# Optimization experiments

Hardware: AMD Instinct MI355X
Metric: run time of the kernel (lower is better)

Reference implementation:

```python
import jax, jax.numpy as jnp
import numpy as np

B, S, D, H, E = 2, 512, 768, 12, 8
FF = 4 * D
HD = D // H


def setup_inputs() -> dict:
    key = jax.random.key(0)
    ks = jax.random.split(key, 12)
    s = 0.02
    return {
        "x": jax.random.normal(ks[0], (B, S, D), jnp.float32),
        "ln1_g": jnp.ones((D,), jnp.float32),
        "ln1_b": jnp.zeros((D,), jnp.float32),
        "ln2_g": jnp.ones((D,), jnp.float32),
        "ln2_b": jnp.zeros((D,), jnp.float32),
        "in_proj_w": jax.random.normal(ks[1], (3 * D, D), jnp.float32) * s,
        "in_proj_b": jax.random.normal(ks[2], (3 * D,), jnp.float32) * s,
        "out_proj_w": jax.random.normal(ks[3], (D, D), jnp.float32) * s,
        "out_proj_b": jax.random.normal(ks[4], (D,), jnp.float32) * s,
        "router_w": jax.random.normal(ks[5], (E, D), jnp.float32) * s,
        "router_b": jax.random.normal(ks[6], (E,), jnp.float32) * s,
        "w1": jax.random.normal(ks[7], (E, D, FF), jnp.float32) * s,
        "b1": jax.random.normal(ks[8], (E, FF), jnp.float32) * s,
        "w2": jax.random.normal(ks[9], (E, FF, D), jnp.float32) * s,
        "b2": jax.random.normal(ks[10], (E, D), jnp.float32) * s,
    }


def _layernorm(x, g, b, eps=1e-5):
    mu = x.mean(-1, keepdims=True)
    var = ((x - mu) ** 2).mean(-1, keepdims=True)
    return (x - mu) * jax.lax.rsqrt(var + eps) * g + b


def _forward(x, ln1_g, ln1_b, ln2_g, ln2_b, in_proj_w, in_proj_b,
             out_proj_w, out_proj_b, router_w, router_b, w1, b1, w2, b2):
    # --- self-attention sublayer (pre-norm per torch module ordering) ---
    h = _layernorm(x, ln1_g, ln1_b)
    qkv = h @ in_proj_w.T + in_proj_b                     # [B,S,3D]
    q, k, v = jnp.split(qkv, 3, axis=-1)
    to_heads = lambda t: t.reshape(B, S, H, HD).transpose(0, 2, 1, 3)  # [B,H,S,hd]
    q, k, v = to_heads(q), to_heads(k), to_heads(v)
    scores = jnp.einsum('bhqd,bhkd->bhqk', q, k) / np.float32(np.sqrt(HD))
    attn = jax.nn.softmax(scores, axis=-1)
    o = jnp.einsum('bhqk,bhkd->bhqd', attn, v).transpose(0, 2, 1, 3).reshape(B, S, D)
    o = o @ out_proj_w.T + out_proj_b
    x = x + o
    # --- MoE sublayer: top-2 routing, renormalized gates ---
    h2 = _layernorm(x, ln2_g, ln2_b)
    t = h2.reshape(-1, D)                                  # [T,D]
    logits = t @ router_w.T + router_b                     # [T,E]
    probs = jax.nn.softmax(logits, axis=-1)
    top_v, top_i = jax.lax.top_k(probs, 2)                 # [T,2]
    top_v = top_v / top_v.sum(-1, keepdims=True)
    # per-(token, expert) combine weight (0 if expert not in token's top-2)
    comb = jnp.sum(jax.nn.one_hot(top_i, E, dtype=probs.dtype) * top_v[..., None], axis=1)  # [T,E]
    # dense grouped-FFN: every token through every expert, zero-weighted combine
    hid = jax.nn.gelu(jnp.einsum('td,edf->tef', t, w1) + b1, approximate=False)  # exact GELU as torch
    y = jnp.einsum('tef,efd->ted', hid, w2) + b2           # [T,E,D]
    moe = jnp.einsum('te,ted->td', comb, y).reshape(B, S, D)
    return x + moe


def reference(x, ln1_g, ln1_b, ln2_g, ln2_b, in_proj_w, in_proj_b,
              out_proj_w, out_proj_b, router_w, router_b, w1, b1, w2, b2):
    return _forward(x, ln1_g, ln1_b, ln2_g, ln2_b, in_proj_w, in_proj_b,
                    out_proj_w, out_proj_b, router_w, router_b, w1, b1, w2, b2)
```

## Files before the change

### kernel.cpp

```cpp
#include <hip/hip_runtime.h>
#include <hip/hip_bf16.h>

#define BATCH 2
#define SEQ 512
#define DIM 768
#define HEADS 12
#define NEXP 8
#define FFDIM 3072
#define HDIM 64
#define NTOK (BATCH*SEQ)
#define NENT (2*NTOK)
#define YPS ((long)NENT * DIM)

typedef __hip_bfloat16 bf16;
typedef __attribute__((ext_vector_type(8))) short s8v;
typedef __attribute__((ext_vector_type(4))) float f4v;

typedef __attribute__((address_space(1))) const unsigned char gas_u8;
typedef __attribute__((address_space(3))) unsigned char las_u8;
__device__ __forceinline__ void gload16(const void* g, void* l) {
    __builtin_amdgcn_global_load_lds((gas_u8*)g, (las_u8*)l, 16, 0, 0);
}

__device__ __forceinline__ float bfbits2f(unsigned hi16) {
    union { unsigned u; float f; } c; c.u = hi16; return c.f;
}
__device__ __forceinline__ unsigned short bf16bits(float f) {
    bf16 h = __float2bfloat16(f);
    return *reinterpret_cast<unsigned short*>(&h);
}

__global__ __launch_bounds__(256) void ln_kernel(const float* __restrict__ x,
                                                 const float* __restrict__ g,
                                                 const float* __restrict__ b,
                                                 bf16* __restrict__ outb) {
    int t = blockIdx.x;
    const float* xr = x + (long)t * DIM;
    int tid = threadIdx.x;
    float v0 = xr[tid], v1 = xr[tid + 256], v2 = xr[tid + 512];
    float s = v0 + v1 + v2;
    __shared__ float red[4];
    #pragma unroll
    for (int o = 32; o; o >>= 1) s += __shfl_xor(s, o);
    if ((tid & 63) == 0) red[tid >> 6] = s;
    __syncthreads();
    s = red[0] + red[1] + red[2] + red[3];
    float mu = s * (1.f / DIM);
    float d0 = v0 - mu, d1 = v1 - mu, d2 = v2 - mu;
    float q = d0*d0 + d1*d1 + d2*d2;
    __shared__ float red2[4];
    #pragma unroll
    for (int o = 32; o; o >>= 1) q += __shfl_xor(q, o);
    if ((tid & 63) == 0) red2[tid >> 6] = q;
    __syncthreads();
    q = red2[0] + red2[1] + red2[2] + red2[3];
    float rstd = rsqrtf(q * (1.f / DIM) + 1e-5f);
    bf16* ob = outb + (long)t * DIM;
    ob[tid]       = __float2bfloat16(d0 * rstd * g[tid]       + b[tid]);
    ob[tid + 256] = __float2bfloat16(d1 * rstd * g[tid + 256] + b[tid + 256]);
    ob[tid + 512] = __float2bfloat16(d2 * rstd * g[tid + 512] + b[tid + 512]);
}

__global__ __launch_bounds__(256) void ln2x1_kernel(const float* __restrict__ x,
                                                    const float* __restrict__ out_b,
                                                    const float* __restrict__ op,
                                                    const float* __restrict__ g,
                                                    const float* __restrict__ b,
                                                    float* __restrict__ x1,
                                                    float* __restrict__ t2,
                                                    bf16* __restrict__ t2b) {
    int t = blockIdx.x;
    long base = (long)t * DIM;
    int tid = threadIdx.x;
    const long TDl = (long)NTOK * DIM;
    float v[3];
    #pragma unroll
    for (int i = 0; i < 3; ++i) {
        long idx = base + tid + i * 256;
        v[i] = x[idx] + out_b[tid + i * 256] + op[idx] + op[idx + TDl];
        x1[idx] = v[i];
    }
    float s = v[0] + v[1] + v[2];
    __shared__ float red[4];
    #pragma unroll
    for (int o = 32; o; o >>= 1) s += __shfl_xor(s, o);
    if ((tid & 63) == 0) red[tid >> 6] = s;
    __syncthreads();
    s = red[0] + red[1] + red[2] + red[3];
    float mu = s * (1.f / DIM);
    float d[3];
    float q = 0.f;
    #pragma unroll
    for (int i = 0; i < 3; ++i) { d[i] = v[i] - mu; q += d[i] * d[i]; }
    __shared__ float red2[4];
    #pragma unroll
    for (int o = 32; o; o >>= 1) q += __shfl_xor(q, o);
    if ((tid & 63) == 0) red2[tid >> 6] = q;
    __syncthreads();
    q = red2[0] + red2[1] + red2[2] + red2[3];
    float rstd = rsqrtf(q * (1.f / DIM) + 1e-5f);
    #pragma unroll
    for (int i = 0; i < 3; ++i) {
        long idx = base + tid + i * 256;
        float o = d[i] * rstd * g[tid + i * 256] + b[tid + i * 256];
        t2[idx] = o;
        t2b[idx] = __float2bfloat16(o);
    }
}

template<int WM, int WN, bool GROUPED, bool GELU, int OUTMODE>
__global__ __launch_bounds__(256) void mfma_gemm(
    const bf16* __restrict__ A, const bf16* __restrict__ B,
    const float* __restrict__ bias, const float* __restrict__ resid,
    void* __restrict__ Cv,
    int M, int N, int K, int lda, int ldb, int ldc,
    int zdiv, int ksplit,
    long a_hi, long a_lo, long b_hi, long b_lo, long c_hi, long c_lo,
    long bias_stride, const int* __restrict__ grp_off, float alpha)
{
    constexpr int BM = 32 * WM, BN = 32 * WN;
    constexpr int ACH = BM * 4;
    constexpr int BCH = BN * 4;

    int z = blockIdx.z;
    int ze = z / ksplit, ks = z % ksplit;
    int kper = K / ksplit;
    long aoff, boff, coff;
    int m_count = M;
    if (GROUPED) {
        int m0 = grp_off[ze], m1 = grp_off[ze + 1];
        m_count = m1 - m0;
        if ((int)blockIdx.y * BM >= m_count) return;
        aoff = (long)m0 * lda;
        coff = (long)m0 * ldc;
        boff = (long)ze * b_hi;
    } else {
        int zh = ze / zdiv, zl = ze % zdiv;
        aoff = zh * a_hi + zl * a_lo;
        boff = zh * b_hi + zl * b_lo;
        coff = zh * c_hi + zl * c_lo;
    }
    const short* Ag = (const short*)(A + aoff);
    const short* Bg = (const short*)(B + boff);
    const float* biasp = bias ? bias + (long)ze * bias_stride : nullptr;
    float* Cf = (float*)Cv + coff;
    bf16*  Cb = (bf16*)Cv + coff;

    __shared__ short As[BM * 32];
    __shared__ short Bs[BN * 32];

    int tid = threadIdx.x;
    int wv = tid >> 6, ln = tid & 63;
    int wr = wv >> 1, wc = wv & 1;
    int fr = ln & 15, fq = ln >> 4;
    int bm = blockIdx.y * BM, bn = blockIdx.x * BN;

    f4v acc[WM][WN] = {};

    for (int k0 = ks * kper; k0 < (ks + 1) * kper; k0 += 32) {
        #pragma unroll
        for (int is = 0; is < ACH / 256; ++is) {
            int c = is * 256 + wv * 64 + ln;
            int m = c >> 2, kq = c & 3;
            int qg = kq ^ ((m >> 1) & 3);
            gload16(Ag + (long)(bm + m) * lda + k0 + qg * 8,
                    &As[(is * 256 + wv * 64) * 8]);
        }
        if constexpr (ACH % 256) {
            if (tid < ACH % 256) {
                int c = (ACH / 256) * 256 + tid;
                int m = c >> 2, kq = c & 3;
                int qg = kq ^ ((m >> 1) & 3);
                gload16(Ag + (long)(bm + m) * lda + k0 + qg * 8,
                        &As[((ACH / 256) * 256 + wv * 64) * 8]);
            }
        }
        #pragma unroll
        for (int is = 0; is < BCH / 256; ++is) {
            int c = is * 256 + wv * 64 + ln;
            int m = c >> 2, kq = c & 3;
            int qg = kq ^ ((m >> 1) & 3);
            gload16(Bg + (long)(bn + m) * ldb + k0 + qg * 8,
                    &Bs[(is * 256 + wv * 64) * 8]);
        }
        if constexpr (BCH % 256) {
            if (tid < BCH % 256) {
                int c = (BCH / 256) * 256 + tid;
                int m = c >> 2, kq = c & 3;
                int qg = kq ^ ((m >> 1) & 3);
                gload16(Bg + (long)(bn + m) * ldb + k0 + qg * 8,
                        &Bs[((BCH / 256) * 256 + wv * 64) * 8]);
            }
        }
        __syncthreads();
        s8v av[WM], bv[WN];
        #pragma unroll
        for (int i = 0; i < WM; ++i) {
            int row = wr * (WM * 16) + i * 16 + fr;
            av[i] = *(const s8v*)&As[row * 32 + (fq ^ ((row >> 1) & 3)) * 8];
        }
        #pragma unroll
        for (int j = 0; j < WN; ++j) {
            int row = wc * (WN * 16) + j * 16 + fr;
            bv[j] = *(const s8v*)&Bs[row * 32 + (fq ^ ((row >> 1) & 3)) * 8];
        }
        #pragma unroll
        for (int i = 0; i < WM; ++i)
            #pragma unroll
            for (int j = 0; j < WN; ++j)
                acc[i][j] = __builtin_amdgcn_mfma_f32_16x16x32_bf16(av[i], bv[j], acc[i][j], 0, 0, 0);
        __syncthreads();
    }

    #pragma unroll
    for (int i = 0; i < WM; ++i) {
        #pragma unroll
        for (int r = 0; r < 4; ++r) {
            int row = bm + wr * (WM * 16) + i * 16 + fq * 4 + r;
            if (GROUPED && row >= m_count) continue;
            #pragma unroll
            for (int j = 0; j < WN; ++j) {
                int col = bn + wc * (WN * 16) + j * 16 + fr;
                if (col < N) {
                    float v = acc[i][j][r] * alpha;
                    if (OUTMODE == 2) {
                        atomicAdd(&Cf[(long)row * ldc + col], v);
                    } else {
                        if (biasp) v += biasp[col];
                        if (GELU) v = 0.5f * v * (1.f + erff(v * 0.70710678118654752f));
                        if (resid) v += resid[(long)row * ldc + col];
                        if (OUTMODE == 1) Cb[(long)row * ldc + col] = __float2bfloat16(v);
                        else              Cf[(long)row * ldc + col] = v;
                    }
                }
            }
        }
    }
}

template<int FM, int FN, int XT, int YCAP, int KS, bool GELU, int OUTMODE, bool GATHER>
__global__ __launch_bounds__(256) void moe_gemm(
    const bf16* __restrict__ A, const bf16* __restrict__ B,
    const float* __restrict__ bias, void* __restrict__ Cv,
    int lda, int Nt, int ldc, int Ktot, long b_hi, long bias_stride,
    const int* __restrict__ grp_off, const int* __restrict__ entry_tok,
    int N, long pstride)
{
    static_assert(OUTMODE != 1 || KS == 1, "plain bf16 store requires no split-K");
    constexpr int BM = FM * 32, BN = FN * 32;
    constexpr int GA = BM / 64;
    constexpr int GB = BN / 64;
    constexpr int G = GA + GB;

    int bid = blockIdx.x;
    int e = bid & 7;
    int r = bid >> 3;
    int xt = r % XT; r /= XT;
    int yt = r % YCAP;
    int ks = r / YCAP;
    int m0 = grp_off[e], m1 = grp_off[e + 1];
    int m_count = m1 - m0;
    int bm = yt * BM;
    if (bm >= m_count) return;
    int bn = xt * BN;
    int kper = Ktot / KS;

    const short* Ag = (const short*)A + (GATHER ? 0 : (long)m0 * lda);
    const short* Bg = (const short*)(B + (long)e * b_hi);
    const float* biasp = bias ? bias + (long)e * bias_stride : nullptr;
    float* Cf = (float*)Cv + (long)m0 * ldc + (long)ks * pstride;
    bf16*  Cb = (bf16*)Cv + (long)m0 * ldc;

    __shared__ short As[3][BM * 32];
    __shared__ short Bs[3][BN * 32];

    int tid = threadIdx.x;
    int wv = tid >> 6, ln = tid & 63;
    int wr = wv >> 1, wc = wv & 1;
    int fr = ln & 15, fq = ln >> 4;

    long arow[GA];
    #pragma unroll
    for (int is = 0; is < GA; ++is) {
        int c = is * 256 + wv * 64 + ln;
        int m = c >> 2;
        if (GATHER) {
            int gi = m0 + bm + m;
            arow[is] = (long)entry_tok[gi < NENT ? gi : NENT - 1] * lda;
        } else {
            arow[is] = (long)(bm + m) * lda;
        }
    }

    f4v acc[FM][FN] = {};

    auto stage = [&](int buf, int k0) {
        #pragma unroll
        for (int is = 0; is < GA; ++is) {
            int c = is * 256 + wv * 64 + ln;
            int m = c >> 2, q = c & 3;
            int qg = q ^ ((m >> 1) & 3);
            gload16(Ag + arow[is] + k0 + qg * 8,
                    &As[buf][(is * 256 + wv * 64) * 8]);
        }
        #pragma unroll
        for (int is = 0; is < GB; ++is) {
            int c = is * 256 + wv * 64 + ln;
            int n = c >> 2, q = c & 3;
            int qg = q ^ ((n >> 1) & 3);
            gload16(Bg + ((long)(k0 >> 3) + qg) * Nt * 8 + (long)(bn + n) * 8,
                    &Bs[buf][(is * 256 + wv * 64) * 8]);
        }
    };

    int kbeg = ks * kper;
    int nit = kper / 32;
    stage(0, kbeg);
    if (nit > 1) stage(1, kbeg + 32);

    for (int it = 0; it < nit; ++it) {
        if (it + 1 < nit) asm volatile("s_waitcnt vmcnt(%0)" :: "i"(G) : "memory");
        else              asm volatile("s_waitcnt vmcnt(0)" ::: "memory");
        __builtin_amdgcn_s_barrier();
        if (it + 2 < nit) stage((it + 2) % 3, kbeg + (it + 2) * 32);
        int cur = it % 3;
        __builtin_amdgcn_s_setprio(1);
        {
            s8v av[FM], bv[FN];
            #pragma unroll
            for (int i = 0; i < FM; ++i) {
                int row = wr * (FM * 16) + i * 16 + fr;
                av[i] = *(const s8v*)&As[cur][row * 32 + (fq ^ ((row >> 1) & 3)) * 8];
            }
            #pragma unroll
            for (int j = 0; j < FN; ++j) {
                int row = wc * (FN * 16) + j * 16 + fr;
                bv[j] = *(const s8v*)&Bs[cur][row * 32 + (fq ^ ((row >> 1) & 3)) * 8];
            }
            #pragma unroll
            for (int i = 0; i < FM; ++i)
                #pragma unroll
                for (int j = 0; j < FN; ++j)
                    acc[i][j] = __builtin_amdgcn_mfma_f32_16x16x32_bf16(av[i], bv[j], acc[i][j], 0, 0, 0);
        }
        __builtin_amdgcn_s_setprio(0);
    }

    #pragma unroll
    for (int i = 0; i < FM; ++i) {
        #pragma unroll
        for (int rr = 0; rr < 4; ++rr) {
            int row = bm + wr * (FM * 16) + i * 16 + fq * 4 + rr;
            if (row >= m_count) continue;
            #pragma unroll
            for (int j = 0; j < FN; ++j) {
                int col = bn + wc * (FN * 16) + j * 16 + fr;
                float v = acc[i][j][rr];
                if (OUTMODE == 0) {
                    Cf[(long)row * ldc + col] = v;
                } else {
                    if (biasp) v += biasp[col];
                    if (GELU) v = 0.5f * v * (1.f + erff(v * 0.70710678118654752f));
                    Cb[(long)row * ldc + col] = __float2bfloat16(v);
                }
            }
        }
    }
}

__global__ __launch_bounds__(256) void softmax512b(const bf16* __restrict__ s,
                                                   bf16* __restrict__ attn) {
    long row = (long)blockIdx.x * 4 + (threadIdx.x >> 6);
    int ln = threadIdx.x & 63;
    const unsigned* p = (const unsigned*)(s + row * 512);
    uint4 v = *(const uint4*)(p + ln * 4);
    unsigned u[4] = {v.x, v.y, v.z, v.w};
    float f[8];
    #pragma unroll
    for (int j = 0; j < 4; ++j) {
        f[2*j]   = bfbits2f(u[j] << 16);
        f[2*j+1] = bfbits2f(u[j] & 0xffff0000u);
    }
    float m = f[0];
    #pragma unroll
    for (int j = 1; j < 8; ++j) m = fmaxf(m, f[j]);
    #pragma unroll
    for (int o = 32; o; o >>= 1) m = fmaxf(m, __shfl_xor(m, o));
    float e[8], ssum = 0.f;
    #pragma unroll
    for (int j = 0; j < 8; ++j) { e[j] = expf(f[j] - m); ssum += e[j]; }
    #pragma unroll
    for (int o = 32; o; o >>= 1) ssum += __shfl_xor(ssum, o);
    float inv = 1.f / ssum;
    unsigned w[4];
    #pragma unroll
    for (int j = 0; j < 4; ++j) {
        bf16 lo = __float2bfloat16(e[2*j] * inv);
        bf16 hi = __float2bfloat16(e[2*j+1] * inv);
        w[j] = ((unsigned)*(unsigned short*)&hi << 16) | *(unsigned short*)&lo;
    }
    uint4 o4; o4.x = w[0]; o4.y = w[1]; o4.z = w[2]; o4.w = w[3];
    *(uint4*)((unsigned*)(attn + row * 512) + ln * 4) = o4;
}

__global__ __launch_bounds__(256) void vt_kernel(const bf16* __restrict__ qkvb,
                                                 bf16* __restrict__ vt) {
    int st = blockIdx.x;
    int z = blockIdx.y;
    int b = z / HEADS, h = z % HEADS;
    __shared__ short tile[64][65];
    int t = threadIdx.x;
    int d = t & 63, s0 = t >> 6;
    const short* q = (const short*)qkvb;
    #pragma unroll
    for (int i = 0; i < 16; ++i) {
        int s = st * 64 + s0 + i * 4;
        tile[s0 + i * 4][d] = q[(long)(b * SEQ + s) * 2304 + 2 * DIM + h * HDIM + d];
    }
    __syncthreads();
    short* o = (short*)vt;
    #pragma unroll
    for (int i = 0; i < 16; ++i) {
        int d2 = (t >> 6) + i * 4;
        o[(long)(z * 64 + d2) * 512 + st * 64 + (t & 63)] = tile[t & 63][d2];
    }
}

__global__ __launch_bounds__(256) void wtrans2_kernel(const float* __restrict__ w1,
                                                      bf16* __restrict__ w1t,
                                                      const float* __restrict__ w2,
                                                      bf16* __restrict__ w2t) {
    int id = blockIdx.x;
    const float* in; bf16* out; int C, e, ct, rt;
    if (id < 4608) {
        e = id / 576; int rem = id % 576; ct = rem / 12; rt = rem % 12;
        in = w1; out = w1t; C = FFDIM;
    } else {
        id -= 4608;
        e = id / 576; int rem = id % 576; ct = rem / 48; rt = rem % 48;
        in = w2; out = w2t; C = DIM;
    }
    long ibase = (long)e * DIM * FFDIM;
    int rt0 = rt * 64, ct0 = ct * 64;
    __shared__ float tile[64][65];
    int t = threadIdx.x;
    {
        int q = t >> 4, cq = t & 15;
        #pragma unroll
        for (int i = 0; i < 4; ++i) {
            int row = q + i * 16;
            float4 v = *(const float4*)&in[ibase + (long)(rt0 + row) * C + ct0 + cq * 4];
            tile[row][cq * 4]     = v.x;
            tile[row][cq * 4 + 1] = v.y;
            tile[row][cq * 4 + 2] = v.z;
            tile[row][cq * 4 + 3] = v.w;
        }
    }
    __syncthreads();
    {
        int kb2 = t >> 6, n = t & 63;
        #pragma unroll
        for (int i = 0; i < 2; ++i) {
            int kblk = kb2 + 4 * i;
            unsigned w[4];
            #pragma unroll
            for (int j = 0; j < 4; ++j) {
                w[j] = ((unsigned)bf16bits(tile[kblk * 8 + 2 * j + 1][n]) << 16)
                     | bf16bits(tile[kblk * 8 + 2 * j][n]);
            }
            uint4 u; u.x = w[0]; u.y = w[1]; u.z = w[2]; u.w = w[3];
            *(uint4*)&out[ibase + ((long)(rt0 >> 3) + kblk) * C * 8 + (long)(ct0 + n) * 8] = u;
        }
    }
}

__global__ __launch_bounds__(256) void cvt2_kernel(const float* __restrict__ a, long na,
                                                   const float* __restrict__ b, long nb,
                                                   bf16* __restrict__ oa,
                                                   bf16* __restrict__ ob) {
    long i = ((long)blockIdx.x * 256 + threadIdx.x) * 4;
    const float* src; bf16* dst; long idx;
    if (i < na) { src = a; dst = oa; idx = i; }
    else if (i < na + nb) { src = b; dst = ob; idx = i - na; }
    else return;
    float4 v = *(const float4*)(src + idx);
    dst[idx]     = __float2bfloat16(v.x);
    dst[idx + 1] = __float2bfloat16(v.y);
    dst[idx + 2] = __float2bfloat16(v.z);
    dst[idx + 3] = __float2bfloat16(v.w);
}

__global__ __launch_bounds__(64) void router_kernel(const float* __restrict__ t2,
                                                    const float* __restrict__ rw,
                                                    const float* __restrict__ rb,
                                                    int* __restrict__ e_sel,
                                                    float* __restrict__ w_sel) {
    int t = blockIdx.x;
    int lane = threadIdx.x;
    const float* tr = t2 + (long)t * DIM;
    float tv[12];
    #pragma unroll
    for (int i = 0; i < 12; ++i) tv[i] = tr[lane + 64 * i];
    float logits[NEXP];
    #pragma unroll
    for (int e = 0; e < NEXP; ++e) {
        const float* wr = rw + (long)e * DIM;
        float s = 0.f;
        #pragma unroll
        for (int i = 0; i < 12; ++i) s += tv[i] * wr[lane + 64 * i];
        #pragma unroll
        for (int o = 32; o; o >>= 1) s += __shfl_xor(s, o);
        logits[e] = s + rb[e];
    }
    if (lane == 0) {
        int e0 = -1, e1 = -1;
        float l0 = -1e30f, l1 = -1e30f;
        #pragma unroll
        for (int e = 0; e < NEXP; ++e) {
            float l = logits[e];
            if (l > l0) { l1 = l0; e1 = e0; l0 = l; e0 = e; }
            else if (l > l1) { l1 = l; e1 = e; }
        }
        float p1 = expf(l1 - l0);
        float inv = 1.f / (1.f + p1);
        e_sel[t * 2] = e0;  e_sel[t * 2 + 1] = e1;
        w_sel[t * 2] = inv; w_sel[t * 2 + 1] = p1 * inv;
    }
}

__global__ __launch_bounds__(1024) void build_lists(const int* __restrict__ e_sel,
                                                    int* __restrict__ entry_tok,
                                                    int* __restrict__ pos,
                                                    int* __restrict__ grp_off) {
    __shared__ int cnt[NEXP];
    __shared__ int off[NEXP + 1];
    __shared__ int cur[NEXP];
    int tid = threadIdx.x;
    if (tid < NEXP) cnt[tid] = 0;
    __syncthreads();
    for (int i = tid; i < NENT; i += 1024) atomicAdd(&cnt[e_sel[i]], 1);
    __syncthreads();
    if (tid == 0) {
        off[0] = 0;
        for (int e = 0; e < NEXP; ++e) off[e + 1] = off[e] + cnt[e];
        for (int e = 0; e < NEXP; ++e) cur[e] = off[e];
    }
    __syncthreads();
    for (int i = tid; i < NENT; i += 1024) {
        int e = e_sel[i];
        int p = atomicAdd(&cur[e], 1);
        entry_tok[p] = i >> 1;
        pos[i] = p;
    }
    if (tid < NEXP + 1) grp_off[tid] = off[tid];
}

__global__ __launch_bounds__(256) void combine_kernel(const float* __restrict__ x1,
                                                      const float* __restrict__ ypart,
                                                      const float* __restrict__ b2,
                                                      const int* __restrict__ pos,
                                                      const int* __restrict__ e_sel,
                                                      const float* __restrict__ wsel,
                                                      float* __restrict__ out) {
    long i4 = (long)blockIdx.x * 256 + threadIdx.x;
    if (i4 >= (long)NTOK * DIM / 4) return;
    int t = (int)(i4 / 192), d4 = (int)(i4 % 192);
    const float4* x1v = (const float4*)x1;
    const float4* ypv = (const float4*)ypart;
    const float4* b2v = (const float4*)b2;
    float4 v = x1v[i4];
    #pragma unroll
    for (int s = 0; s < 2; ++s) {
        long base = (long)pos[t * 2 + s] * 192 + d4;
        float4 y = b2v[(long)e_sel[t * 2 + s] * 192 + d4];
        #pragma unroll
        for (int ks = 0; ks < 4; ++ks) {
            float4 pp = ypv[base + ks * (YPS / 4)];
            y.x += pp.x; y.y += pp.y; y.z += pp.z; y.w += pp.w;
        }
        float w = wsel[t * 2 + s];
        v.x += w * y.x; v.y += w * y.y; v.z += w * y.z; v.w += w * y.w;
    }
    ((float4*)out)[i4] = v;
}

extern "C" void kernel_launch(void* const* d_in, const int* in_sizes, int n_in,
                              void* d_out, int out_size, void* d_ws, size_t ws_size,
                              hipStream_t stream) {
    const float* x        = (const float*)d_in[0];
    const float* ln1_g    = (const float*)d_in[1];
    const float* ln1_b    = (const float*)d_in[2];
    const float* ln2_g    = (const float*)d_in[3];
    const float* ln2_b    = (const float*)d_in[4];
    const float* in_w     = (const float*)d_in[5];
    const float* in_b     = (const float*)d_in[6];
    const float* out_w    = (const float*)d_in[7];
    const float* out_b    = (const float*)d_in[8];
    const float* router_w = (const float*)d_in[9];
    const float* router_b = (const float*)d_in[10];
    const float* w1       = (const float*)d_in[11];
    const float* b1       = (const float*)d_in[12];
    const float* w2       = (const float*)d_in[13];
    const float* b2       = (const float*)d_in[14];
    float* out = (float*)d_out;

    const long TD = (long)NTOK * DIM;
    char* p = (char*)d_ws;
    size_t off = 0;
    auto alloc = [&](size_t bytes) -> void* {
        void* r = p + off; off += (bytes + 255) & ~(size_t)255; return r;
    };
    bf16*  h_b    = (bf16*)alloc(TD * 2);
    bf16*  in_wb  = (bf16*)alloc(2304L * 768 * 2);
    bf16*  qkv_b  = (bf16*)alloc(1024L * 2304 * 2);
    bf16*  out_wb = (bf16*)alloc(768L * 768 * 2);
    bf16*  vt_b   = (bf16*)alloc((24L * 64 + 64) * 512 * 2);
    bf16*  oat_b  = (bf16*)alloc(TD * 2);
    float* opart  = (float*)alloc(2 * TD * 4);
    float* x1     = (float*)alloc(TD * 4);
    float* t2     = (float*)alloc(TD * 4);
    bf16*  t2b    = (bf16*)alloc((NTOK + 256L) * DIM * 2);
    bf16*  w1t    = (bf16*)alloc(8L * 3072 * 768 * 2);
    bf16*  w2t    = (bf16*)alloc(8L * 768 * 3072 * 2);
    bf16*  hid    = (bf16*)alloc((2048L + 256) * 3072 * 2);
    float* ypart  = (float*)alloc(4 * YPS * 4);
    int*   e_sel     = (int*)alloc(NENT * 4);
    float* w_sel     = (float*)alloc(NENT * 4);
    int*   entry_tok = (int*)alloc(NENT * 4);
    int*   pos       = (int*)alloc(NENT * 4);
    int*   grp_off   = (int*)alloc(64);
    bf16* scores = w1t;
    bf16* attn   = (bf16*)((char*)w1t + 24L * 512 * 512 * 2);

    ln_kernel<<<NTOK, 256, 0, stream>>>(x, ln1_g, ln1_b, h_b);
    cvt2_kernel<<<2304, 256, 0, stream>>>(in_w, 2304L * 768, out_w, 768L * 768,
                                          in_wb, out_wb);
    mfma_gemm<2, 2, false, false, 1><<<dim3(36, 16, 1), 256, 0, stream>>>(
        h_b, in_wb, in_b, nullptr, qkv_b,
        NTOK, 3 * DIM, DIM, DIM, DIM, 3 * DIM,
        1, 1, 0, 0, 0, 0, 0, 0, 0, nullptr, 1.f);
    mfma_gemm<2, 4, false, false, 1><<<dim3(4, 8, 24), 256, 0, stream>>>(
        qkv_b, qkv_b + DIM, nullptr, nullptr, scores,
        SEQ, SEQ, HDIM, 3 * DIM, 3 * DIM, SEQ,
        HEADS, 1, (long)SEQ * 3 * DIM, HDIM, (long)SEQ * 3 * DIM, HDIM,
        (long)HEADS * SEQ * SEQ, (long)SEQ * SEQ,
        0, nullptr, 0.125f);
    softmax512b<<<24 * SEQ / 4, 256, 0, stream>>>(scores, attn);
    vt_kernel<<<dim3(8, 24), 256, 0, stream>>>(qkv_b, vt_b);
    mfma_gemm<1, 2, false, false, 1><<<dim3(1, 16, 24), 256, 0, stream>>>(
        attn, vt_b, nullptr, nullptr, oat_b,
        SEQ, HDIM, SEQ, SEQ, SEQ, DIM,
        HEADS, 1, (long)HEADS * SEQ * SEQ, (long)SEQ * SEQ,
        (long)HEADS * HDIM * SEQ, (long)HDIM * SEQ,
        (long)SEQ * DIM, HDIM,
        0, nullptr, 1.f);
    mfma_gemm<2, 2, false, false, 0><<<dim3(12, 16, 2), 256, 0, stream>>>(
        oat_b, out_wb, nullptr, nullptr, opart,
        NTOK, DIM, 384, DIM, DIM, DIM,
        2, 1, 0, 384, 0, 384, 0, TD, 0, nullptr, 1.f);
    ln2x1_kernel<<<NTOK, 256, 0, stream>>>(x, out_b, opart, ln2_g, ln2_b,
                                           x1, t2, t2b);
    router_kernel<<<NTOK, 64, 0, stream>>>(t2, router_w, router_b, e_sel, w_sel);
    build_lists<<<1, 1024, 0, stream>>>(e_sel, entry_tok, pos, grp_off);
    wtrans2_kernel<<<9216, 256, 0, stream>>>(w1, w1t, w2, w2t);
    moe_gemm<4, 4, 24, 8, 1, true, 1, true><<<8 * 24 * 8, 256, 0, stream>>>(
        t2b, w1t, b1, hid,
        DIM, FFDIM, FFDIM, DIM, (long)FFDIM * DIM, FFDIM, grp_off, entry_tok,
        FFDIM, 0);
    moe_gemm<4, 4, 6, 8, 4, false, 0, false><<<8 * 6 * 8 * 4, 256, 0, stream>>>(
        hid, w2t, nullptr, ypart,
        FFDIM, DIM, DIM, FFDIM, (long)FFDIM * DIM, 0, grp_off, nullptr,
        DIM, YPS);
    combine_kernel<<<768, 256, 0, stream>>>(x1, ypart, b2, pos, e_sel, w_sel, out);
}
```

Before: 187.8 us.

## Co-schedule expert weight transpose with QKV and score GEMMs in fused launches

Turns the GEMM kernel into a device function that takes explicit block indices and shared memory, then builds two combined kernels. One runs the QKV projection blocks next to the w1 transpose blocks, the other runs the attention-score GEMM blocks next to the w2 transpose blocks. The aim is to fill idle compute units during the small attention GEMMs with the memory-bound weight conversion and to remove a separate launch. Scores and attention now get their own buffers instead of aliasing w1t, which costs extra workspace memory. The fused kernels reserve the larger shared-memory size for every block, which may lower occupancy.

```diff
diff --git a/kernel.cpp b/kernel.cpp
--- a/kernel.cpp
+++ b/kernel.cpp
@@ -109,20 +109,21 @@
 }
 
 template<int WM, int WN, bool GROUPED, bool GELU, int OUTMODE>
-__global__ __launch_bounds__(256) void mfma_gemm(
+__device__ __forceinline__ void dev_mfma_gemm(
     const bf16* __restrict__ A, const bf16* __restrict__ B,
     const float* __restrict__ bias, const float* __restrict__ resid,
     void* __restrict__ Cv,
     int M, int N, int K, int lda, int ldb, int ldc,
     int zdiv, int ksplit,
     long a_hi, long a_lo, long b_hi, long b_lo, long c_hi, long c_lo,
-    long bias_stride, const int* __restrict__ grp_off, float alpha)
+    long bias_stride, const int* __restrict__ grp_off, float alpha,
+    int bx, int by, int bz, char* smem)
 {
     constexpr int BM = 32 * WM, BN = 32 * WN;
     constexpr int ACH = BM * 4;
     constexpr int BCH = BN * 4;
 
-    int z = blockIdx.z;
+    int z = bz;
     int ze = z / ksplit, ks = z % ksplit;
     int kper = K / ksplit;
     long aoff, boff, coff;
@@ -130,7 +131,7 @@
     if (GROUPED) {
         int m0 = grp_off[ze], m1 = grp_off[ze + 1];
         m_count = m1 - m0;
-        if ((int)blockIdx.y * BM >= m_count) return;
+        if (by * BM >= m_count) return;
         aoff = (long)m0 * lda;
         coff = (long)m0 * ldc;
         boff = (long)ze * b_hi;
@@ -146,14 +147,14 @@
     float* Cf = (float*)Cv + coff;
     bf16*  Cb = (bf16*)Cv + coff;
 
-    __shared__ short As[BM * 32];
-    __shared__ short Bs[BN * 32];
+    short* As = (short*)smem;
+    short* Bs = As + BM * 32;
 
     int tid = threadIdx.x;
     int wv = tid >> 6, ln = tid & 63;
     int wr = wv >> 1, wc = wv & 1;
     int fr = ln & 15, fq = ln >> 4;
-    int bm = blockIdx.y * BM, bn = blockIdx.x * BN;
+    int bm = by * BM, bn = bx * BN;
 
     f4v acc[WM][WN] = {};
 
@@ -235,6 +236,107 @@
                 }
             }
         }
+    }
+}
+
+template<int WM, int WN, bool GROUPED, bool GELU, int OUTMODE>
+__global__ __launch_bounds__(256) void mfma_gemm(
+    const bf16* A, const bf16* B, const float* bias, const float* resid,
+    void* Cv, int M, int N, int K, int lda, int ldb, int ldc,
+    int zdiv, int ksplit,
+    long a_hi, long a_lo, long b_hi, long b_lo, long c_hi, long c_lo,
+    long bias_stride, const int* grp_off, float alpha)
+{
+    __shared__ char smem[(32 * WM + 32 * WN) * 32 * 2];
+    dev_mfma_gemm<WM, WN, GROUPED, GELU, OUTMODE>(
+        A, B, bias, resid, Cv, M, N, K, lda, ldb, ldc, zdiv, ksplit,
+        a_hi, a_lo, b_hi, b_lo, c_hi, c_lo, bias_stride, grp_off, alpha,
+        blockIdx.x, blockIdx.y, blockIdx.z, smem);
+}
+
+__device__ __forceinline__ void dev_wtrans(int id,
+                                           const float* __restrict__ w1,
+                                           bf16* __restrict__ w1t,
+                                           const float* __restrict__ w2,
+                                           bf16* __restrict__ w2t,
+                                           char* smem) {
+    const float* in; bf16* out; int C, e, ct, rt;
+    if (id < 4608) {
+        e = id / 576; int rem = id % 576; ct = rem / 12; rt = rem % 12;
+        in = w1; out = w1t; C = FFDIM;
+    } else {
+        id -= 4608;
+        e = id / 576; int rem = id % 576; ct = rem / 48; rt = rem % 48;
+        in = w2; out = w2t; C = DIM;
+    }
+    long ibase = (long)e * DIM * FFDIM;
+    int rt0 = rt * 64, ct0 = ct * 64;
+    float (*tile)[65] = (float(*)[65])smem;
+    int t = threadIdx.x;
+    {
+        int q = t >> 4, cq = t & 15;
+        #pragma unroll
+        for (int i = 0; i < 4; ++i) {
+            int row = q + i * 16;
+            float4 v = *(const float4*)&in[ibase + (long)(rt0 + row) * C + ct0 + cq * 4];
+            tile[row][cq * 4]     = v.x;
+            tile[row][cq * 4 + 1] = v.y;
+            tile[row][cq * 4 + 2] = v.z;
+            tile[row][cq * 4 + 3] = v.w;
+        }
+    }
+    __syncthreads();
+    {
+        int kb2 = t >> 6, n = t & 63;
+        #pragma unroll
+        for (int i = 0; i < 2; ++i) {
+            int kblk = kb2 + 4 * i;
+            unsigned w[4];
+            #pragma unroll
+            for (int j = 0; j < 4; ++j) {
+                w[j] = ((unsigned)bf16bits(tile[kblk * 8 + 2 * j + 1][n]) << 16)
+                     | bf16bits(tile[kblk * 8 + 2 * j][n]);
+            }
+            uint4 u; u.x = w[0]; u.y = w[1]; u.z = w[2]; u.w = w[3];
+            *(uint4*)&out[ibase + ((long)(rt0 >> 3) + kblk) * C * 8 + (long)(ct0 + n) * 8] = u;
+        }
+    }
+}
+
+__global__ __launch_bounds__(256) void qkv_w1_kernel(
+    const bf16* __restrict__ h_b, const bf16* __restrict__ in_wb,
+    const float* __restrict__ in_b, bf16* __restrict__ qkv_b,
+    const float* __restrict__ w1, bf16* __restrict__ w1t,
+    const float* __restrict__ w2, bf16* __restrict__ w2t) {
+    __shared__ char smem[16640];
+    int bid = blockIdx.x;
+    if (bid < 576) {
+        dev_mfma_gemm<2, 2, false, false, 1>(
+            h_b, in_wb, in_b, nullptr, qkv_b,
+            NTOK, 3 * DIM, DIM, DIM, DIM, 3 * DIM,
+            1, 1, 0, 0, 0, 0, 0, 0, 0, nullptr, 1.f,
+            bid % 36, bid / 36, 0, smem);
+    } else {
+        dev_wtrans(bid - 576, w1, w1t, w2, w2t, smem);
+    }
+}
+
+__global__ __launch_bounds__(256) void scores_w2_kernel(
+    const bf16* __restrict__ qkv_b, bf16* __restrict__ scores,
+    const float* __restrict__ w1, bf16* __restrict__ w1t,
+    const float* __restrict__ w2, bf16* __restrict__ w2t) {
+    __shared__ char smem[16640];
+    int bid = blockIdx.x;
+    if (bid < 768) {
+        dev_mfma_gemm<2, 4, false, false, 1>(
+            qkv_b, qkv_b + DIM, nullptr, nullptr, scores,
+            SEQ, SEQ, HDIM, 3 * DIM, 3 * DIM, SEQ,
+            HEADS, 1, (long)SEQ * 3 * DIM, HDIM, (long)SEQ * 3 * DIM, HDIM,
+            (long)HEADS * SEQ * SEQ, (long)SEQ * SEQ,
+            0, nullptr, 0.125f,
+            bid % 4, (bid >> 2) & 7, bid >> 5, smem);
+    } else {
+        dev_wtrans(4608 + (bid - 768), w1, w1t, w2, w2t, smem);
     }
 }
 
@@ -426,54 +528,6 @@
     }
 }
 
-__global__ __launch_bounds__(256) void wtrans2_kernel(const float* __restrict__ w1,
-                                                      bf16* __restrict__ w1t,
-                                                      const float* __restrict__ w2,
-                                                      bf16* __restrict__ w2t) {
-    int id = blockIdx.x;
-    const float* in; bf16* out; int C, e, ct, rt;
-    if (id < 4608) {
-        e = id / 576; int rem = id % 576; ct = rem / 12; rt = rem % 12;
-        in = w1; out = w1t; C = FFDIM;
-    } else {
-        id -= 4608;
-        e = id / 576; int rem = id % 576; ct = rem / 48; rt = rem % 48;
-        in = w2; out = w2t; C = DIM;
-    }
-    long ibase = (long)e * DIM * FFDIM;
-    int rt0 = rt * 64, ct0 = ct * 64;
-    __shared__ float tile[64][65];
-    int t = threadIdx.x;
-    {
-        int q = t >> 4, cq = t & 15;
-        #pragma unroll
-        for (int i = 0; i < 4; ++i) {
-            int row = q + i * 16;
-            float4 v = *(const float4*)&in[ibase + (long)(rt0 + row) * C + ct0 + cq * 4];
-            tile[row][cq * 4]     = v.x;
-            tile[row][cq * 4 + 1] = v.y;
-            tile[row][cq * 4 + 2] = v.z;
-            tile[row][cq * 4 + 3] = v.w;
-        }
-    }
-    __syncthreads();
-    {
-        int kb2 = t >> 6, n = t & 63;
-        #pragma unroll
-        for (int i = 0; i < 2; ++i) {
-            int kblk = kb2 + 4 * i;
-            unsigned w[4];
-            #pragma unroll
-            for (int j = 0; j < 4; ++j) {
-                w[j] = ((unsigned)bf16bits(tile[kblk * 8 + 2 * j + 1][n]) << 16)
-                     | bf16bits(tile[kblk * 8 + 2 * j][n]);
-            }
-            uint4 u; u.x = w[0]; u.y = w[1]; u.z = w[2]; u.w = w[3];
-            *(uint4*)&out[ibase + ((long)(rt0 >> 3) + kblk) * C * 8 + (long)(ct0 + n) * 8] = u;
-        }
-    }
-}
-
 __global__ __launch_bounds__(256) void cvt2_kernel(const float* __restrict__ a, long na,
                                                    const float* __restrict__ b, long nb,
                                                    bf16* __restrict__ oa,
@@ -622,6 +676,8 @@
     bf16*  t2b    = (bf16*)alloc((NTOK + 256L) * DIM * 2);
     bf16*  w1t    = (bf16*)alloc(8L * 3072 * 768 * 2);
     bf16*  w2t    = (bf16*)alloc(8L * 768 * 3072 * 2);
+    bf16*  scores = (bf16*)alloc(24L * 512 * 512 * 2);
+    bf16*  attn   = (bf16*)alloc(24L * 512 * 512 * 2);
     bf16*  hid    = (bf16*)alloc((2048L + 256) * 3072 * 2);
     float* ypart  = (float*)alloc(4 * YPS * 4);
     int*   e_sel     = (int*)alloc(NENT * 4);
@@ -629,22 +685,14 @@
     int*   entry_tok = (int*)alloc(NENT * 4);
     int*   pos       = (int*)alloc(NENT * 4);
     int*   grp_off   = (int*)alloc(64);
-    bf16* scores = w1t;
-    bf16* attn   = (bf16*)((char*)w1t + 24L * 512 * 512 * 2);
 
     ln_kernel<<<NTOK, 256, 0, stream>>>(x, ln1_g, ln1_b, h_b);
     cvt2_kernel<<<2304, 256, 0, stream>>>(in_w, 2304L * 768, out_w, 768L * 768,
                                           in_wb, out_wb);
-    mfma_gemm<2, 2, false, false, 1><<<dim3(36, 16, 1), 256, 0, stream>>>(
-        h_b, in_wb, in_b, nullptr, qkv_b,
-        NTOK, 3 * DIM, DIM, DIM, DIM, 3 * DIM,
-        1, 1, 0, 0, 0, 0, 0, 0, 0, nullptr, 1.f);
-    mfma_gemm<2, 4, false, false, 1><<<dim3(4, 8, 24), 256, 0, stream>>>(
-        qkv_b, qkv_b + DIM, nullptr, nullptr, scores,
-        SEQ, SEQ, HDIM, 3 * DIM, 3 * DIM, SEQ,
-        HEADS, 1, (long)SEQ * 3 * DIM, HDIM, (long)SEQ * 3 * DIM, HDIM,
-        (long)HEADS * SEQ * SEQ, (long)SEQ * SEQ,
-        0, nullptr, 0.125f);
+    qkv_w1_kernel<<<576 + 4608, 256, 0, stream>>>(h_b, in_wb, in_b, qkv_b,
+                                                  w1, w1t, w2, w2t);
+    scores_w2_kernel<<<768 + 4608, 256, 0, stream>>>(qkv_b, scores,
+                                                     w1, w1t, w2, w2t);
     softmax512b<<<24 * SEQ / 4, 256, 0, stream>>>(scores, attn);
     vt_kernel<<<dim3(8, 24), 256, 0, stream>>>(qkv_b, vt_b);
     mfma_gemm<1, 2, false, false, 1><<<dim3(1, 16, 24), 256, 0, stream>>>(
@@ -662,7 +710,6 @@
                                            x1, t2, t2b);
     router_kernel<<<NTOK, 64, 0, stream>>>(t2, router_w, router_b, e_sel, w_sel);
     build_lists<<<1, 1024, 0, stream>>>(e_sel, entry_tok, pos, grp_off);
-    wtrans2_kernel<<<9216, 256, 0, stream>>>(w1, w1t, w2, w2t);
     moe_gemm<4, 4, 24, 8, 1, true, 1, true><<<8 * 24 * 8, 256, 0, stream>>>(
         t2b, w1t, b1, hid,
         DIM, FFDIM, FFDIM, DIM, (long)FFDIM * DIM, FFDIM, grp_off, entry_tok,
```

Measured after the change: 185.6 us. About the same (-1.2%).
